# Kernel tuning notes

Measured on AMD Instinct MI355X. Metric: run time of the kernel, lower is better.

Reference implementation:

```python
import jax, jax.numpy as jnp
import numpy as np
from jax import lax

EPS = 1e-5
NUM_GROUPS = 32
OFFSET_SCALE = 1.0
K = 3            # deformable conv kernel size
KK = K * K
DWK = 7          # depthwise kernel size for offset predictor


def group_norm(x, gamma, beta, num_groups=NUM_GROUPS):
    B, C, H, W = x.shape
    xg = x.reshape(B, num_groups, C // num_groups, H, W)
    m = xg.mean(axis=(2, 3, 4), keepdims=True)
    v = xg.var(axis=(2, 3, 4), keepdims=True)
    xn = ((xg - m) * lax.rsqrt(v + EPS)).reshape(B, C, H, W)
    return xn * gamma[None, :, None, None] + beta[None, :, None, None]


def bilinear_gather(x, py, px):
    # x: [B,C,H,W]; py, px: [B,KK,H,W] absolute sample coords -> [B,C,KK,H,W]
    B, C, H, W = x.shape
    y0 = jnp.floor(py)
    x0 = jnp.floor(px)
    wy1 = py - y0
    wx1 = px - x0
    wy0 = 1.0 - wy1
    wx0 = 1.0 - wx1
    xf = x.reshape(B, C, H * W)

    def gather(yi, xi):
        valid = (yi >= 0) & (yi <= H - 1) & (xi >= 0) & (xi <= W - 1)
        yc = jnp.clip(yi, 0, H - 1).astype(jnp.int32)
        xc = jnp.clip(xi, 0, W - 1).astype(jnp.int32)
        idx = (yc * W + xc).reshape(B, -1)                      # [B, KK*H*W]
        g = jax.vmap(lambda a, i: a[:, i])(xf, idx)             # [B, C, KK*H*W]
        g = g.reshape(B, C, KK, H, W)
        return g * valid.astype(x.dtype)[:, None]

    out = (gather(y0, x0) * (wy0 * wx0)[:, None]
           + gather(y0, x0 + 1.0) * (wy0 * wx1)[:, None]
           + gather(y0 + 1.0, x0) * (wy1 * wx0)[:, None]
           + gather(y0 + 1.0, x0 + 1.0) * (wy1 * wx1)[:, None])
    return out


def deform_conv(x, dw, pw, pwb, w, b):
    # x: [B,C,H,W]; dw: [C,1,DWK,DWK] depthwise; pw: [2*KK,C,1,1]; w: [O,C,K,K]
    B, C, H, W = x.shape
    dn = ('NCHW', 'OIHW', 'NCHW')
    f = lax.conv_general_dilated(x, dw, (1, 1), 'SAME',
                                 feature_group_count=C, dimension_numbers=dn)
    off = lax.conv_general_dilated(f, pw, (1, 1), 'SAME', dimension_numbers=dn)
    off = (off + pwb[None, :, None, None]) * OFFSET_SCALE       # [B,2*KK,H,W]
    off = off.reshape(B, KK, 2, H, W)
    ks = jnp.arange(K, dtype=x.dtype) - (K - 1) / 2             # [-1,0,1]
    ky = jnp.repeat(ks, K)                                      # [KK]
    kx = jnp.tile(ks, K)
    yy, xx = jnp.meshgrid(jnp.arange(H, dtype=x.dtype),
                          jnp.arange(W, dtype=x.dtype), indexing='ij')
    py = yy[None, None] + ky[None, :, None, None] + off[:, :, 0]  # [B,KK,H,W]
    px = xx[None, None] + kx[None, :, None, None] + off[:, :, 1]
    sampled = bilinear_gather(x, py, px)                        # [B,C,KK,H,W]
    O = w.shape[0]
    out = jnp.einsum('bckhw,ock->bohw', sampled, w.reshape(O, C, KK))
    return out + b[None, :, None, None]


def setup_inputs() -> dict:
    key = jax.random.key(0)
    ks = jax.random.split(key, 10)
    B, C, H, W = 4, 256, 64, 64
    O = C
    x = jax.random.normal(ks[0], (B, C, H, W), dtype=jnp.float32)

    def conv_w(k, shape, fan_in):
        return jax.random.normal(k, shape, dtype=jnp.float32) / np.sqrt(fan_in)

    inp = {
        'x': x,
        'gn1_g': jnp.ones((C,), jnp.float32), 'gn1_b': jnp.zeros((C,), jnp.float32),
        'dw1': conv_w(ks[1], (C, 1, DWK, DWK), DWK * DWK),
        'pw1': jax.random.normal(ks[2], (2 * KK, C, 1, 1), jnp.float32) * 0.01,
        'pwb1': jnp.zeros((2 * KK,), jnp.float32),
        'w1': conv_w(ks[3], (O, C, K, K), C * KK),
        'b1': jnp.zeros((O,), jnp.float32),
        'gn2_g': jnp.ones((O,), jnp.float32), 'gn2_b': jnp.zeros((O,), jnp.float32),
        'dw2': conv_w(ks[4], (O, 1, DWK, DWK), DWK * DWK),
        'pw2': jax.random.normal(ks[5], (2 * KK, O, 1, 1), jnp.float32) * 0.01,
        'pwb2': jnp.zeros((2 * KK,), jnp.float32),
        'w2': conv_w(ks[6], (O, O, K, K), O * KK),
        'b2': jnp.zeros((O,), jnp.float32),
    }
    return inp


def reference(x, gn1_g, gn1_b, dw1, pw1, pwb1, w1, b1,
              gn2_g, gn2_b, dw2, pw2, pwb2, w2, b2):
    h = jax.nn.relu(group_norm(x, gn1_g, gn1_b))
    h = deform_conv(h, dw1, pw1, pwb1, w1, b1)
    h = jax.nn.relu(group_norm(h, gn2_g, gn2_b))
    # Dropout / DropPath are identity in eval mode
    h = deform_conv(h, dw2, pw2, pwb2, w2, b2)
    return h + x  # shortcut is Identity (in_channels == out_channels)
```

## Files before the change

kernel.cpp:

```cpp
#include <hip/hip_runtime.h>

#define B_    4
#define C_    256
#define H_    64
#define W_    64
#define HW_   4096
#define NG_   32
#define CPG_  8
#define KK_   9
#define NOFF_ 18

typedef __attribute__((ext_vector_type(8))) short short8;
typedef __attribute__((ext_vector_type(4))) short short4v;
typedef __attribute__((ext_vector_type(4))) float floatx4;

static __device__ __forceinline__ short f2bf(float f) {
    union { float f; unsigned u; } v; v.f = f;
    unsigned r = v.u + 0x7fff + ((v.u >> 16) & 1);
    return (short)(r >> 16);
}
static __device__ __forceinline__ float bf2f(short s) {
    union { unsigned u; float f; } v;
    v.u = ((unsigned)(unsigned short)s) << 16;
    return v.f;
}

__global__ __launch_bounds__(1024) void gn_relu_kernel(
    const float* __restrict__ in, const float* __restrict__ gamma,
    const float* __restrict__ beta, short* __restrict__ outb)
{
    int b = blockIdx.x >> 5;
    int g = blockIdx.x & 31;
    const int N = CPG_ * HW_;
    size_t base = ((size_t)(b * C_ + g * CPG_)) * HW_;
    const float4* in4 = (const float4*)(in + base);
    int t = threadIdx.x;

    float s = 0.f, ss = 0.f;
    for (int i = t; i < N / 4; i += 1024) {
        float4 v = in4[i];
        s  += v.x + v.y + v.z + v.w;
        ss += v.x * v.x + v.y * v.y + v.z * v.z + v.w * v.w;
    }
    #pragma unroll
    for (int off = 32; off > 0; off >>= 1) {
        s  += __shfl_down(s, off, 64);
        ss += __shfl_down(ss, off, 64);
    }
    __shared__ float red[32];
    __shared__ float sh_rs, sh_m;
    int wid = t >> 6;
    if ((t & 63) == 0) { red[wid] = s; red[16 + wid] = ss; }
    __syncthreads();
    if (t == 0) {
        float S = 0.f, SS = 0.f;
        #pragma unroll
        for (int i = 0; i < 16; ++i) { S += red[i]; SS += red[16 + i]; }
        float m = S / (float)N;
        float var = SS / (float)N - m * m;
        sh_rs = rsqrtf(var + 1e-5f);
        sh_m = m;
    }
    __syncthreads();
    float rs = sh_rs, m = sh_m;
    short4v* out4 = (short4v*)(outb + base);
    for (int i = t; i < N / 4; i += 1024) {
        int ch = g * CPG_ + (i >> 10);
        float ga = gamma[ch] * rs;
        float be = beta[ch] - m * ga;
        float4 v = in4[i];
        short4v o;
        o.x = f2bf(fmaxf(fmaf(v.x, ga, be), 0.f));
        o.y = f2bf(fmaxf(fmaf(v.y, ga, be), 0.f));
        o.z = f2bf(fmaxf(fmaf(v.z, ga, be), 0.f));
        o.w = f2bf(fmaxf(fmaf(v.w, ga, be), 0.f));
        out4[i] = o;
    }
}

__global__ __launch_bounds__(256) void dw7t_kernel(
    const short* __restrict__ in, const float* __restrict__ dwk,
    short* __restrict__ fdw, short* __restrict__ hbt)
{
    int plane = blockIdx.x;
    int b = plane >> 8;
    int c = plane & (C_ - 1);
    const short* src = in + (size_t)plane * HW_;
    __shared__ float tile[70 * 72];
    __shared__ float wk[49];
    int t = threadIdx.x;
    if (t < 49) wk[t] = dwk[c * 49 + t];
    for (int i = t; i < 70 * 72; i += 256) tile[i] = 0.f;
    __syncthreads();
    const short4v* src4 = (const short4v*)src;
    short* hb = hbt + ((size_t)b * HW_) * C_ + c;
    for (int i = t; i < HW_ / 4; i += 256) {
        short4v v = src4[i];
        int y = i >> 4, x = (i & 15) * 4;
        float* tp = &tile[(y + 3) * 72 + (x + 3)];
        tp[0] = bf2f(v.x); tp[1] = bf2f(v.y);
        tp[2] = bf2f(v.z); tp[3] = bf2f(v.w);
        int px = i * 4;
        hb[(size_t)px * C_]       = v.x;
        hb[(size_t)(px + 1) * C_] = v.y;
        hb[(size_t)(px + 2) * C_] = v.z;
        hb[(size_t)(px + 3) * C_] = v.w;
    }
    __syncthreads();
    short* fb = fdw + ((size_t)b * HW_) * C_ + c;
    #pragma unroll
    for (int it = 0; it < 4; ++it) {
        int idx = it * 256 + t;
        int y = idx >> 4;
        int x0 = (idx & 15) * 4;
        float a0 = 0.f, a1 = 0.f, a2 = 0.f, a3 = 0.f;
        #pragma unroll
        for (int dy = 0; dy < 7; ++dy) {
            const float* tr = &tile[(y + dy) * 72 + x0];
            float4 ra = *(const float4*)tr;
            float4 rb = *(const float4*)(tr + 4);
            float4 rc = *(const float4*)(tr + 8);
            float r[12] = {ra.x, ra.y, ra.z, ra.w,
                           rb.x, rb.y, rb.z, rb.w,
                           rc.x, rc.y, rc.z, rc.w};
            const float* wr = &wk[dy * 7];
            #pragma unroll
            for (int dx = 0; dx < 7; ++dx) {
                float wv = wr[dx];
                a0 = fmaf(r[dx], wv, a0);
                a1 = fmaf(r[dx + 1], wv, a1);
                a2 = fmaf(r[dx + 2], wv, a2);
                a3 = fmaf(r[dx + 3], wv, a3);
            }
        }
        size_t ob = (size_t)(y * 64 + x0) * C_;
        fb[ob]          = f2bf(a0);
        fb[ob + C_]     = f2bf(a1);
        fb[ob + 2 * C_] = f2bf(a2);
        fb[ob + 3 * C_] = f2bf(a3);
    }
}

__global__ __launch_bounds__(256) void wpack_all_kernel(
    const float* __restrict__ w1, const float* __restrict__ w2,
    const float* __restrict__ pw1, const float* __restrict__ pw2,
    short* __restrict__ wp1, short* __restrict__ wp2,
    short* __restrict__ ppk1, short* __restrict__ ppk2)
{
    int blk = blockIdx.x;
    if (blk < 4608) {
        const float* w = (blk < 2304) ? w1 : w2;
        short* wp = (blk < 2304) ? wp1 : wp2;
        int idx = (blk & 2047) * 256 + ((blk & 2048) ? 524288 : 0) + threadIdx.x;
        idx = (blk % 2304) * 256 + threadIdx.x;
        int j    = idx & 7;
        int lane = (idx >> 3) & 63;
        int ot   = (idx >> 9) & 15;
        int slab = idx >> 13;
        int k = slab >> 3, cc = slab & 7;
        int o = ot * 16 + (lane & 15);
        int c = cc * 32 + (lane >> 4) * 8 + j;
        wp[idx] = f2bf(w[(size_t)(o * C_ + c) * KK_ + k]);
    } else {
        int q = blk - 4608;
        const float* pw = (q < 32) ? pw1 : pw2;
        short* ppk = (q < 32) ? ppk1 : ppk2;
        int idx = (q & 31) * 256 + threadIdx.x;
        int j = idx & 7, lane = (idx >> 3) & 63;
        int ot = (idx >> 9) & 1, sl = idx >> 10;
        int o = ot * 16 + (lane & 15);
        int k = sl * 32 + (lane >> 4) * 8 + j;
        ppk[idx] = (o < NOFF_) ? f2bf(pw[o * C_ + k]) : (short)0;
    }
}

__global__ __launch_bounds__(1024) void deform_fused_kernel(
    const short* __restrict__ ht,   const short* __restrict__ fdw,
    const short* __restrict__ ppk,  const float* __restrict__ pwb,
    const short* __restrict__ wp,   const float* __restrict__ bias,
    const float* __restrict__ resid, float* __restrict__ out)
{
    int b = blockIdx.x >> 6;
    int row = blockIdx.x & 63;
    __shared__ int   i00[576], i01[576], i10[576], i11[576];
    __shared__ float c00[576], c01[576], c10[576], c11[576];
    __shared__ float off_lds[NOFF_ * 64];
    __shared__ __align__(16) short sbuf[2][16384];
    int t = threadIdx.x;
    int wv = t >> 6, lane = t & 63;
    int pq = lane >> 4, pr = lane & 15;

    if (wv < 8) {
        int ot = wv & 1, ptw = wv >> 1;
        int px = ptw * 16 + pr;
        const short8* fb8 = (const short8*)(fdw +
            ((size_t)b * HW_ + row * 64 + px) * C_);
        const short8* ap = (const short8*)ppk;
        floatx4 pacc = (floatx4){0.f, 0.f, 0.f, 0.f};
        #pragma unroll
        for (int sl = 0; sl < 8; ++sl) {
            short8 af = ap[(sl * 2 + ot) * 64 + lane];
            short8 bf = fb8[sl * 4 + pq];
            pacc = __builtin_amdgcn_mfma_f32_16x16x32_bf16(af, bf, pacc, 0, 0, 0);
        }
        #pragma unroll
        for (int r = 0; r < 4; ++r) {
            int o = ot * 16 + pq * 4 + r;
            if (o < NOFF_) off_lds[o * 64 + px] = pacc[r] + pwb[o];
        }
    }
    __syncthreads();

    if (t < 576) {
        int e = t;
        int k = e >> 6, p = e & 63;
        float offy = off_lds[(2 * k) * 64 + p];
        float offx = off_lds[(2 * k + 1) * 64 + p];
        float py = (float)row + (float)(k / 3 - 1) + offy;
        float px = (float)p   + (float)(k % 3 - 1) + offx;
        float y0f = floorf(py), x0f = floorf(px);
        float wy1 = py - y0f, wx1 = px - x0f;
        float wy0 = 1.f - wy1, wx0 = 1.f - wx1;
        float y1f = y0f + 1.f, x1f = x0f + 1.f;
        bool vy0 = (y0f >= 0.f) && (y0f <= 63.f);
        bool vy1 = (y1f >= 0.f) && (y1f <= 63.f);
        bool vx0 = (x0f >= 0.f) && (x0f <= 63.f);
        bool vx1 = (x1f >= 0.f) && (x1f <= 63.f);
        int iy0 = (int)fminf(fmaxf(y0f, 0.f), 63.f);
        int iy1 = (int)fminf(fmaxf(y1f, 0.f), 63.f);
        int ix0 = (int)fminf(fmaxf(x0f, 0.f), 63.f);
        int ix1 = (int)fminf(fmaxf(x1f, 0.f), 63.f);
        i00[e] = iy0 * 64 + ix0; i01[e] = iy0 * 64 + ix1;
        i10[e] = iy1 * 64 + ix0; i11[e] = iy1 * 64 + ix1;
        c00[e] = (vy0 && vx0) ? wy0 * wx0 : 0.f;
        c01[e] = (vy0 && vx1) ? wy0 * wx1 : 0.f;
        c10[e] = (vy1 && vx0) ? wy1 * wx0 : 0.f;
        c11[e] = (vy1 && vx1) ? wy1 * wx1 : 0.f;
    }
    __syncthreads();

    int scb = t & 3, spx = (t >> 2) & 63, ssl0 = t >> 8;
    int u2 = spx * 4 + (scb ^ ((spx + (spx >> 2)) & 3));
    const short* hb = ht + ((size_t)b * HW_) * C_;
    const short* hb0 = hb + ssl0 * 32 + scb * 8;
    const short* hb1 = hb + (ssl0 + 4) * 32 + scb * 8;

    short8 ra[4], rb[4];
    auto prefetch = [&](int g) {
        int e = g * 64 + spx;
        int a00 = i00[e], a01 = i01[e], a10 = i10[e], a11 = i11[e];
        ra[0] = *(const short8*)(hb0 + (size_t)a00 * C_);
        ra[1] = *(const short8*)(hb0 + (size_t)a01 * C_);
        ra[2] = *(const short8*)(hb0 + (size_t)a10 * C_);
        ra[3] = *(const short8*)(hb0 + (size_t)a11 * C_);
        rb[0] = *(const short8*)(hb1 + (size_t)a00 * C_);
        rb[1] = *(const short8*)(hb1 + (size_t)a01 * C_);
        rb[2] = *(const short8*)(hb1 + (size_t)a10 * C_);
        rb[3] = *(const short8*)(hb1 + (size_t)a11 * C_);
    };
    auto stage_write = [&](int g, int bi) {
        int e = g * 64 + spx;
        float w00 = c00[e], w01 = c01[e], w10 = c10[e], w11 = c11[e];
        short8 va, vb;
        #pragma unroll
        for (int j = 0; j < 8; ++j) {
            va[j] = f2bf(w00 * bf2f(ra[0][j]) + w01 * bf2f(ra[1][j])
                       + w10 * bf2f(ra[2][j]) + w11 * bf2f(ra[3][j]));
            vb[j] = f2bf(w00 * bf2f(rb[0][j]) + w01 * bf2f(rb[1][j])
                       + w10 * bf2f(rb[2][j]) + w11 * bf2f(rb[3][j]));
        }
        *(short8*)&sbuf[bi][ssl0 * 2048 + u2 * 8] = va;
        *(short8*)&sbuf[bi][(ssl0 + 4) * 2048 + u2 * 8] = vb;
    };

    floatx4 acc[4];
    #pragma unroll
    for (int pt = 0; pt < 4; ++pt) acc[pt] = (floatx4){0.f, 0.f, 0.f, 0.f};
    int ub[4];
    #pragma unroll
    for (int pt = 0; pt < 4; ++pt) {
        int px2 = pt * 16 + pr;
        ub[pt] = px2 * 4 + (pq ^ ((px2 + (px2 >> 2)) & 3));
    }

    prefetch(0);
    stage_write(0, 0);
    prefetch(1);
    __syncthreads();

    const short8* wp8 = (const short8*)wp;
    for (int g = 0; g < 9; ++g) {
        const short* sb = sbuf[g & 1];
        #pragma unroll
        for (int half = 0; half < 2; ++half) {
            short8 af[4];
            #pragma unroll
            for (int q = 0; q < 4; ++q)
                af[q] = wp8[(size_t)((g * 8 + half * 4 + q) * 16 + wv) * 64 + lane];
            #pragma unroll
            for (int q = 0; q < 4; ++q) {
                int sl = half * 4 + q;
                #pragma unroll
                for (int pt = 0; pt < 4; ++pt) {
                    short8 bfv = *(const short8*)&sb[sl * 2048 + ub[pt] * 8];
                    acc[pt] = __builtin_amdgcn_mfma_f32_16x16x32_bf16(
                        af[q], bfv, acc[pt], 0, 0, 0);
                }
            }
        }
        if (g + 1 < 9) {
            stage_write(g + 1, (g + 1) & 1);
            if (g + 2 < 9) prefetch(g + 2);
        }
        __syncthreads();
    }

    #pragma unroll
    for (int r = 0; r < 4; ++r) {
        int o = wv * 16 + pq * 4 + r;
        float bo = bias[o];
        size_t obase = ((size_t)(b * C_ + o)) * HW_ + row * 64 + pr;
        #pragma unroll
        for (int pt = 0; pt < 4; ++pt) {
            float v = acc[pt][r] + bo;
            if (resid) v += resid[obase + pt * 16];
            out[obase + pt * 16] = v;
        }
    }
}

extern "C" void kernel_launch(void* const* d_in, const int* in_sizes, int n_in,
                              void* d_out, int out_size, void* d_ws, size_t ws_size,
                              hipStream_t stream)
{
    const float* x     = (const float*)d_in[0];
    const float* gn1_g = (const float*)d_in[1];
    const float* gn1_b = (const float*)d_in[2];
    const float* dw1   = (const float*)d_in[3];
    const float* pw1   = (const float*)d_in[4];
    const float* pwb1  = (const float*)d_in[5];
    const float* w1    = (const float*)d_in[6];
    const float* b1    = (const float*)d_in[7];
    const float* gn2_g = (const float*)d_in[8];
    const float* gn2_b = (const float*)d_in[9];
    const float* dw2   = (const float*)d_in[10];
    const float* pw2   = (const float*)d_in[11];
    const float* pwb2  = (const float*)d_in[12];
    const float* w2    = (const float*)d_in[13];
    const float* b2    = (const float*)d_in[14];
    float* out = (float*)d_out;

    float* ws   = (float*)d_ws;
    float* y1   = ws;
    short* hbf  = (short*)(ws + 4194304);
    short* hbt  = (short*)(ws + 6291456);
    short* fdw  = (short*)(ws + 8388608);
    short* wp1  = (short*)(ws + 10485760);
    short* wp2  = (short*)(ws + 10780672);
    short* ppk1 = (short*)(ws + 11075584);
    short* ppk2 = (short*)(ws + 11079680);

    wpack_all_kernel<<<4672, 256, 0, stream>>>(w1, w2, pw1, pw2,
                                               wp1, wp2, ppk1, ppk2);

    gn_relu_kernel<<<B_ * NG_, 1024, 0, stream>>>(x, gn1_g, gn1_b, hbf);
    dw7t_kernel<<<B_ * C_, 256, 0, stream>>>(hbf, dw1, fdw, hbt);
    deform_fused_kernel<<<B_ * H_, 1024, 0, stream>>>(
        hbt, fdw, ppk1, pwb1, wp1, b1, nullptr, y1);

    gn_relu_kernel<<<B_ * NG_, 1024, 0, stream>>>(y1, gn2_g, gn2_b, hbf);
    dw7t_kernel<<<B_ * C_, 256, 0, stream>>>(hbf, dw2, fdw, hbt);
    deform_fused_kernel<<<B_ * H_, 1024, 0, stream>>>(
        hbt, fdw, ppk2, pwb2, wp2, b2, x, out);
}
```

Baseline: 291.7 us.

## Split transposes into a coalesced LDS tile kernel and store intermediate in bf16

The depthwise kernel used to write both the NHWC copy of its input and its output as strided 2-byte scatters with a stride of C. It now writes NCHW output with vector stores, and a separate transpose kernel swizzles both tensors through LDS into NHWC with 16-byte coalesced writes. The first deform conv's output is also stored as bf16 instead of fp32, and a bf16 GroupNorm variant reads it, halving that round trip. The cost is one extra launch plus an extra read and write of two tensors, and some precision lost in the intermediate activation.

Measured after the change: 250.5 us. 14.1% less time.

```diff
diff --git a/kernel.cpp b/kernel.cpp
--- a/kernel.cpp
+++ b/kernel.cpp
@@ -25,7 +25,7 @@
     return v.f;
 }
 
-__global__ __launch_bounds__(1024) void gn_relu_kernel(
+__global__ __launch_bounds__(1024) void gn_relu_f32_kernel(
     const float* __restrict__ in, const float* __restrict__ gamma,
     const float* __restrict__ beta, short* __restrict__ outb)
 {
@@ -78,14 +78,68 @@
     }
 }
 
-__global__ __launch_bounds__(256) void dw7t_kernel(
+__global__ __launch_bounds__(1024) void gn_relu_bf16_kernel(
+    const short* __restrict__ in, const float* __restrict__ gamma,
+    const float* __restrict__ beta, short* __restrict__ outb)
+{
+    int b = blockIdx.x >> 5;
+    int g = blockIdx.x & 31;
+    const int N = CPG_ * HW_;
+    size_t base = ((size_t)(b * C_ + g * CPG_)) * HW_;
+    const short4v* in4 = (const short4v*)(in + base);
+    int t = threadIdx.x;
+
+    float s = 0.f, ss = 0.f;
+    for (int i = t; i < N / 4; i += 1024) {
+        short4v sv = in4[i];
+        float vx = bf2f(sv.x), vy = bf2f(sv.y), vz = bf2f(sv.z), vw = bf2f(sv.w);
+        s  += vx + vy + vz + vw;
+        ss += vx * vx + vy * vy + vz * vz + vw * vw;
+    }
+    #pragma unroll
+    for (int off = 32; off > 0; off >>= 1) {
+        s  += __shfl_down(s, off, 64);
+        ss += __shfl_down(ss, off, 64);
+    }
+    __shared__ float red[32];
+    __shared__ float sh_rs, sh_m;
+    int wid = t >> 6;
+    if ((t & 63) == 0) { red[wid] = s; red[16 + wid] = ss; }
+    __syncthreads();
+    if (t == 0) {
+        float S = 0.f, SS = 0.f;
+        #pragma unroll
+        for (int i = 0; i < 16; ++i) { S += red[i]; SS += red[16 + i]; }
+        float m = S / (float)N;
+        float var = SS / (float)N - m * m;
+        sh_rs = rsqrtf(var + 1e-5f);
+        sh_m = m;
+    }
+    __syncthreads();
+    float rs = sh_rs, m = sh_m;
+    short4v* out4 = (short4v*)(outb + base);
+    for (int i = t; i < N / 4; i += 1024) {
+        int ch = g * CPG_ + (i >> 10);
+        float ga = gamma[ch] * rs;
+        float be = beta[ch] - m * ga;
+        short4v sv = in4[i];
+        short4v o;
+        o.x = f2bf(fmaxf(fmaf(bf2f(sv.x), ga, be), 0.f));
+        o.y = f2bf(fmaxf(fmaf(bf2f(sv.y), ga, be), 0.f));
+        o.z = f2bf(fmaxf(fmaf(bf2f(sv.z), ga, be), 0.f));
+        o.w = f2bf(fmaxf(fmaf(bf2f(sv.w), ga, be), 0.f));
+        out4[i] = o;
+    }
+}
+
+__global__ __launch_bounds__(256) void dw7_kernel(
     const short* __restrict__ in, const float* __restrict__ dwk,
-    short* __restrict__ fdw, short* __restrict__ hbt)
+    short* __restrict__ out)
 {
     int plane = blockIdx.x;
-    int b = plane >> 8;
     int c = plane & (C_ - 1);
     const short* src = in + (size_t)plane * HW_;
+    short* dst = out + (size_t)plane * HW_;
     __shared__ float tile[70 * 72];
     __shared__ float wk[49];
     int t = threadIdx.x;
@@ -93,21 +147,14 @@
     for (int i = t; i < 70 * 72; i += 256) tile[i] = 0.f;
     __syncthreads();
     const short4v* src4 = (const short4v*)src;
-    short* hb = hbt + ((size_t)b * HW_) * C_ + c;
     for (int i = t; i < HW_ / 4; i += 256) {
         short4v v = src4[i];
         int y = i >> 4, x = (i & 15) * 4;
         float* tp = &tile[(y + 3) * 72 + (x + 3)];
         tp[0] = bf2f(v.x); tp[1] = bf2f(v.y);
         tp[2] = bf2f(v.z); tp[3] = bf2f(v.w);
-        int px = i * 4;
-        hb[(size_t)px * C_]       = v.x;
-        hb[(size_t)(px + 1) * C_] = v.y;
-        hb[(size_t)(px + 2) * C_] = v.z;
-        hb[(size_t)(px + 3) * C_] = v.w;
-    }
-    __syncthreads();
-    short* fb = fdw + ((size_t)b * HW_) * C_ + c;
+    }
+    __syncthreads();
     #pragma unroll
     for (int it = 0; it < 4; ++it) {
         int idx = it * 256 + t;
@@ -133,11 +180,49 @@
                 a3 = fmaf(r[dx + 3], wv, a3);
             }
         }
-        size_t ob = (size_t)(y * 64 + x0) * C_;
-        fb[ob]          = f2bf(a0);
-        fb[ob + C_]     = f2bf(a1);
-        fb[ob + 2 * C_] = f2bf(a2);
-        fb[ob + 3 * C_] = f2bf(a3);
+        short4v o;
+        o.x = f2bf(a0); o.y = f2bf(a1); o.z = f2bf(a2); o.w = f2bf(a3);
+        *(short4v*)&dst[y * 64 + x0] = o;
+    }
+}
+
+__global__ __launch_bounds__(256) void transpose2_kernel(
+    const short* __restrict__ srcA, short* __restrict__ dstA,
+    const short* __restrict__ srcB, short* __restrict__ dstB)
+{
+    int blk = blockIdx.x;
+    const short* src = (blk < 256) ? srcA : srcB;
+    short*       dst = (blk < 256) ? dstA : dstB;
+    int q = blk & 255;
+    int b = q >> 6;
+    int px0 = (q & 63) * 64;
+    __shared__ unsigned ltile[64 * 132];
+    int t = threadIdx.x;
+    const short* sb = src + (size_t)b * C_ * HW_;
+
+    int pq4 = t & 15, cphi = t >> 4;
+    #pragma unroll
+    for (int i = 0; i < 8; ++i) {
+        int cp = i * 16 + cphi;
+        const short* r0 = sb + (size_t)(2 * cp) * HW_ + px0 + pq4 * 4;
+        short4v lo = *(const short4v*)r0;
+        short4v hi = *(const short4v*)(r0 + HW_);
+        #pragma unroll
+        for (int j = 0; j < 4; ++j) {
+            int pl = pq4 * 4 + j;
+            unsigned wrd = (unsigned)(unsigned short)lo[j]
+                         | ((unsigned)(unsigned short)hi[j] << 16);
+            ltile[pl * 132 + (cp ^ ((pl & 7) << 2))] = wrd;
+        }
+    }
+    __syncthreads();
+
+    int co = t & 31, ph = t >> 5;
+    #pragma unroll
+    for (int r = 0; r < 8; ++r) {
+        int pl = r * 8 + ph;
+        uint4 v = *(const uint4*)&ltile[pl * 132 + ((co * 4) ^ ((pl & 7) << 2))];
+        *(uint4*)(dst + ((size_t)b * HW_ + px0 + pl) * C_ + co * 8) = v;
     }
 }
 
@@ -151,8 +236,7 @@
     if (blk < 4608) {
         const float* w = (blk < 2304) ? w1 : w2;
         short* wp = (blk < 2304) ? wp1 : wp2;
-        int idx = (blk & 2047) * 256 + ((blk & 2048) ? 524288 : 0) + threadIdx.x;
-        idx = (blk % 2304) * 256 + threadIdx.x;
+        int idx = (blk % 2304) * 256 + threadIdx.x;
         int j    = idx & 7;
         int lane = (idx >> 3) & 63;
         int ot   = (idx >> 9) & 15;
@@ -178,7 +262,8 @@
     const short* __restrict__ ht,   const short* __restrict__ fdw,
     const short* __restrict__ ppk,  const float* __restrict__ pwb,
     const short* __restrict__ wp,   const float* __restrict__ bias,
-    const float* __restrict__ resid, float* __restrict__ out)
+    const float* __restrict__ resid, float* __restrict__ outf,
+    short* __restrict__ outb)
 {
     int b = blockIdx.x >> 6;
     int row = blockIdx.x & 63;
@@ -323,8 +408,12 @@
         #pragma unroll
         for (int pt = 0; pt < 4; ++pt) {
             float v = acc[pt][r] + bo;
-            if (resid) v += resid[obase + pt * 16];
-            out[obase + pt * 16] = v;
+            if (outf) {
+                if (resid) v += resid[obase + pt * 16];
+                outf[obase + pt * 16] = v;
+            } else {
+                outb[obase + pt * 16] = f2bf(v);
+            }
         }
     }
 }
@@ -351,10 +440,11 @@
     float* out = (float*)d_out;
 
     float* ws   = (float*)d_ws;
-    float* y1   = ws;
-    short* hbf  = (short*)(ws + 4194304);
-    short* hbt  = (short*)(ws + 6291456);
-    short* fdw  = (short*)(ws + 8388608);
+    short* y1b  = (short*)ws;
+    short* hbf  = (short*)(ws + 2097152);
+    short* hbt  = (short*)(ws + 4194304);
+    short* fdwc = (short*)(ws + 6291456);
+    short* fdwt = (short*)(ws + 8388608);
     short* wp1  = (short*)(ws + 10485760);
     short* wp2  = (short*)(ws + 10780672);
     short* ppk1 = (short*)(ws + 11075584);
@@ -363,13 +453,15 @@
     wpack_all_kernel<<<4672, 256, 0, stream>>>(w1, w2, pw1, pw2,
                                                wp1, wp2, ppk1, ppk2);
 
-    gn_relu_kernel<<<B_ * NG_, 1024, 0, stream>>>(x, gn1_g, gn1_b, hbf);
-    dw7t_kernel<<<B_ * C_, 256, 0, stream>>>(hbf, dw1, fdw, hbt);
+    gn_relu_f32_kernel<<<B_ * NG_, 1024, 0, stream>>>(x, gn1_g, gn1_b, hbf);
+    dw7_kernel<<<B_ * C_, 256, 0, stream>>>(hbf, dw1, fdwc);
+    transpose2_kernel<<<512, 256, 0, stream>>>(hbf, hbt, fdwc, fdwt);
     deform_fused_kernel<<<B_ * H_, 1024, 0, stream>>>(
-        hbt, fdw, ppk1, pwb1, wp1, b1, nullptr, y1);
-
-    gn_relu_kernel<<<B_ * NG_, 1024, 0, stream>>>(y1, gn2_g, gn2_b, hbf);
-    dw7t_kernel<<<B_ * C_, 256, 0, stream>>>(hbf, dw2, fdw, hbt);
+        hbt, fdwt, ppk1, pwb1, wp1, b1, nullptr, nullptr, y1b);
+
+    gn_relu_bf16_kernel<<<B_ * NG_, 1024, 0, stream>>>(y1b, gn2_g, gn2_b, hbf);
+    dw7_kernel<<<B_ * C_, 256, 0, stream>>>(hbf, dw2, fdwc);
+    transpose2_kernel<<<512, 256, 0, stream>>>(hbf, hbt, fdwc, fdwt);
     deform_fused_kernel<<<B_ * H_, 1024, 0, stream>>>(
-        hbt, fdw, ppk2, pwb2, wp2, b2, x, out);
-}
+        hbt, fdwt, ppk2, pwb2, wp2, b2, x, out, nullptr);
+}
```
